# Kernel tuning notes

Hardware: AMD Instinct MI355X
Metric: run time of the kernel (lower is better)

Reference implementation:

```python
import jax, jax.numpy as jnp
import numpy as np

D = 512; H = 2048; NH = 8; NL = 6; VX = 32000; VY = 32000
B = 256; SX = 15; SY = 17; PAD = 0; DH = D // NH


def _pe_table(seq_len, d):
    pos = np.arange(seq_len, dtype=np.float32)[:, None]
    div = 1.0 / (10000.0 ** (np.arange(0, d, 2, dtype=np.float32) / d))
    pe = np.zeros((seq_len, d), dtype=np.float32)
    pe[:, 0::2] = np.sin(pos * div)
    pe[:, 1::2] = np.cos(pos * div)
    return jnp.asarray(pe)


def _ln(x, g, b, eps=1e-5):
    m = x.mean(-1, keepdims=True)
    v = ((x - m) ** 2).mean(-1, keepdims=True)
    return g * (x - m) / jnp.sqrt(v + eps) + b


def _attn(xq, xkv, mask, w, b):
    # w: [4, D, D] (q,k,v,o), b: [4, D]; mask broadcastable to [B,NH,Sq,Sk]
    bs, sq, _ = xq.shape
    sk = xkv.shape[1]
    q = (xq @ w[0] + b[0]).reshape(bs, sq, NH, DH).transpose(0, 2, 1, 3)
    k = (xkv @ w[1] + b[1]).reshape(bs, sk, NH, DH).transpose(0, 2, 1, 3)
    v = (xkv @ w[2] + b[2]).reshape(bs, sk, NH, DH).transpose(0, 2, 1, 3)
    s = jnp.einsum('bhqd,bhkd->bhqk', q, k) / np.sqrt(float(DH))
    s = jnp.where(mask == 0.0, -1e9, s)
    p = jax.nn.softmax(s, axis=-1)
    o = jnp.einsum('bhqk,bhkd->bhqd', p, v).transpose(0, 2, 1, 3).reshape(bs, sq, D)
    return o @ w[3] + b[3]


def setup_inputs():
    key = jax.random.key(0)
    ks = jax.random.split(key, 24)
    s = 0.02
    x = jax.random.randint(ks[0], (B, SX), 0, VX)
    y = jax.random.randint(ks[1], (B, SY), 0, VY)
    emb_x = (jax.random.normal(ks[2], (VX, D)) * s).at[PAD].set(0.0)
    emb_y = (jax.random.normal(ks[3], (VY, D)) * s).at[PAD].set(0.0)
    inp = dict(x=x, y=y, emb_x=emb_x, emb_y=emb_y)
    inp['enc_attn_w'] = jax.random.normal(ks[4], (NL, 4, D, D)) * s
    inp['enc_attn_b'] = jnp.zeros((NL, 4, D))
    inp['enc_ln'] = jnp.stack([jnp.ones((NL, 2, D)), jnp.zeros((NL, 2, D))], axis=2)  # [NL,2,2,D] (g,b)
    inp['enc_ffn_w0'] = jax.random.normal(ks[5], (NL, D, H)) * s
    inp['enc_ffn_b0'] = jnp.zeros((NL, H))
    inp['enc_ffn_w1'] = jax.random.normal(ks[6], (NL, H, D)) * s
    inp['enc_ffn_b1'] = jnp.zeros((NL, D))
    inp['dec_attn_w'] = jax.random.normal(ks[7], (NL, 8, D, D)) * s  # self q,k,v,o then cross q,k,v,o
    inp['dec_attn_b'] = jnp.zeros((NL, 8, D))
    inp['dec_ln'] = jnp.stack([jnp.ones((NL, 3, D)), jnp.zeros((NL, 3, D))], axis=2)  # [NL,3,2,D]
    inp['dec_ffn_w0'] = jax.random.normal(ks[8], (NL, D, H)) * s
    inp['dec_ffn_b0'] = jnp.zeros((NL, H))
    inp['dec_ffn_w1'] = jax.random.normal(ks[9], (NL, H, D)) * s
    inp['dec_ffn_b1'] = jnp.zeros((NL, D))
    inp['fc_w'] = jax.random.normal(ks[10], (D, VY)) * s
    inp['fc_b'] = jnp.zeros((VY,))
    return inp


def reference(x, y, emb_x, emb_y, enc_attn_w, enc_attn_b, enc_ln,
              enc_ffn_w0, enc_ffn_b0, enc_ffn_w1, enc_ffn_b1,
              dec_attn_w, dec_attn_b, dec_ln,
              dec_ffn_w0, dec_ffn_b0, dec_ffn_w1, dec_ffn_b1,
              fc_w, fc_b):
    pe = _pe_table(max(SX, SY + 1), D)
    mask_x = (x != PAD).astype(jnp.float32)[:, None, None, :]        # [B,1,1,SX]
    mask_pad = (y != PAD).astype(jnp.float32)[:, None, None, :]       # [B,1,1,SY]
    mask_y = mask_pad * jnp.tril(jnp.ones((SY, SY), jnp.float32))     # [B,1,SY,SY]

    hx = emb_x[x] + pe[:SX]
    for i in range(NL):
        a = _attn(hx, hx, mask_x, enc_attn_w[i], enc_attn_b[i])
        h0 = _ln(hx + a, enc_ln[i, 0, 0], enc_ln[i, 0, 1])
        f = jax.nn.relu(h0 @ enc_ffn_w0[i] + enc_ffn_b0[i]) @ enc_ffn_w1[i] + enc_ffn_b1[i]
        hx = _ln(h0 + f, enc_ln[i, 1, 0], enc_ln[i, 1, 1])

    hy = emb_y[y] + pe[:SY]
    for i in range(NL):
        a = _attn(hy, hy, mask_y, dec_attn_w[i, :4], dec_attn_b[i, :4])
        h0 = _ln(hy + a, dec_ln[i, 0, 0], dec_ln[i, 0, 1])
        c = _attn(h0, hx, mask_x, dec_attn_w[i, 4:], dec_attn_b[i, 4:])
        h1 = _ln(h0 + c, dec_ln[i, 1, 0], dec_ln[i, 1, 1])
        f = jax.nn.relu(h1 @ dec_ffn_w0[i] + dec_ffn_b0[i]) @ dec_ffn_w1[i] + dec_ffn_b1[i]
        hy = _ln(h1 + f, dec_ln[i, 2, 0], dec_ln[i, 2, 1])

    return hy @ fc_w + fc_b  # [B, SY, VY]
```

## Files before the change

### kernel.cpp

```cpp
#include <hip/hip_runtime.h>
#include <hip/hip_bf16.h>
#include <stdint.h>
#include <type_traits>

typedef __hip_bfloat16 bf16;
typedef __attribute__((ext_vector_type(8))) short bf16x8;
typedef __attribute__((ext_vector_type(4))) float f32x4;

#define DMODEL 512
#define HFF    2048
#define NHEADS 8
#define NLAYERS 6
#define DHEAD  64
#define BATCH  256
#define SXLEN  15
#define SYLEN  17

__device__ __forceinline__ float us2f(unsigned short u) {
  union { unsigned int i; float f; } c; c.i = ((unsigned int)u) << 16; return c.f;
}
__device__ __forceinline__ unsigned short f2us(float f) {
  bf16 h = __float2bfloat16(f);
  return *reinterpret_cast<unsigned short*>(&h);
}
__device__ __forceinline__ float b2f(bf16 v) { return __bfloat162float(v); }

__device__ __forceinline__ void gload_lds16(const void* g, void* l) {
  __builtin_amdgcn_global_load_lds(
      (const __attribute__((address_space(1))) unsigned int*)g,
      (__attribute__((address_space(3))) unsigned int*)l, 16, 0, 0);
}

template<int RELU, int MT, int NT, int WM, int WN, int ZMAP, int BIAS, typename OT>
__global__ __launch_bounds__(WM * WN * 64) void gemm_t(
    const bf16* __restrict__ A, const bf16* __restrict__ Wt,
    const float* __restrict__ bias, OT* __restrict__ C,
    int M, int N, int K, int ldk,
    long long wStride, long long bStride, long long cStride)
{
  constexpr int BK  = 64;
  constexpr int TH  = WM * WN * 64;
  constexpr int RB  = BK * 2;
  constexpr int MF  = MT / WM / 16;
  constexpr int NF  = NT / WN / 16;
  constexpr int WRS = MT / WM;
  constexpr int WCS = NT / WN;
  constexpr int ABY = MT * RB;
  constexpr int BBY = NT * RB;

  const int z = blockIdx.z;
  long long koff = 0;
  if (ZMAP == 1) {
    int idx = (z >> 1) * 8 + 5 + (z & 1);
    Wt   += (long long)idx * wStride;
    bias += (long long)idx * bStride;
  } else if (ZMAP == 2) {
    koff = (long long)z * K;
  } else {
    Wt   += (long long)z * wStride;
    bias += (long long)z * bStride;
  }
  C += (long long)z * cStride;

  __shared__ __align__(16) char lds[ABY + BBY];
  const int t    = threadIdx.x;
  const int m0   = blockIdx.y * MT, n0 = blockIdx.x * NT;
  const int wid  = t >> 6, lane = t & 63;
  const int wm   = wid / WN, wn = wid % WN;
  const int g    = lane >> 4, r = lane & 15;

  f32x4 acc[MF][NF];
  #pragma unroll
  for (int i = 0; i < MF; ++i)
    #pragma unroll
    for (int j = 0; j < NF; ++j) acc[i][j] = (f32x4)0.f;

  const char* Ab = (const char*)(A  + (long long)m0 * ldk + koff);
  const char* Bb = (const char*)(Wt + (long long)n0 * ldk + koff);
  const int rowBytes = ldk * 2;
  const int rdsw = (r & 7) << 4;

  for (int kt = 0; kt < K; kt += BK) {
    __syncthreads();
    #pragma unroll
    for (int off = 0; off < ABY; off += TH * 16) {
      int o = off + t * 16;
      int row = o >> 7, cb = (o & 127) ^ ((row & 7) << 4);
      gload_lds16(Ab + (long long)row * rowBytes + kt * 2 + cb, lds + o);
    }
    #pragma unroll
    for (int off = 0; off < BBY; off += TH * 16) {
      int o = off + t * 16;
      int row = o >> 7, cb = (o & 127) ^ ((row & 7) << 4);
      gload_lds16(Bb + (long long)row * rowBytes + kt * 2 + cb, lds + ABY + o);
    }
    __syncthreads();

    #pragma unroll
    for (int kh = 0; kh < BK / 32; ++kh) {
      bf16x8 af[MF], bfr[NF];
      #pragma unroll
      for (int ms = 0; ms < MF; ++ms)
        af[ms] = *(const bf16x8*)(lds + (wm * WRS + ms * 16 + r) * RB + ((kh * 64 + g * 16) ^ rdsw));
      #pragma unroll
      for (int ns = 0; ns < NF; ++ns)
        bfr[ns] = *(const bf16x8*)(lds + ABY + (wn * WCS + ns * 16 + r) * RB + ((kh * 64 + g * 16) ^ rdsw));
      #pragma unroll
      for (int ms = 0; ms < MF; ++ms)
        #pragma unroll
        for (int ns = 0; ns < NF; ++ns)
          acc[ms][ns] = __builtin_amdgcn_mfma_f32_16x16x32_bf16(af[ms], bfr[ns], acc[ms][ns], 0, 0, 0);
    }
  }

  #pragma unroll
  for (int ms = 0; ms < MF; ++ms) {
    int rowb = m0 + wm * WRS + ms * 16 + g * 4;
    #pragma unroll
    for (int ns = 0; ns < NF; ++ns) {
      int col = n0 + wn * WCS + ns * 16 + r;
      float bv = BIAS ? bias[col] : 0.f;
      f32x4 v = acc[ms][ns];
      #pragma unroll
      for (int j = 0; j < 4; ++j) {
        float o = v[j] + bv;
        if (RELU) o = fmaxf(o, 0.f);
        if constexpr (std::is_same<OT, float>::value)
          C[(long long)(rowb + j) * N + col] = o;
        else
          C[(long long)(rowb + j) * N + col] = __float2bfloat16(o);
      }
    }
  }
}

__global__ __launch_bounds__(256) void transpose_cast2(
    const float* __restrict__ inA, const float* __restrict__ inB, int zSplit,
    bf16* __restrict__ out, int K, int N)
{
  __shared__ unsigned short tile[32][33];
  int z = blockIdx.z;
  const float* ip = (z < zSplit) ? inA + (long long)z * K * N
                                 : inB + (long long)(z - zSplit) * K * N;
  unsigned short* op = (unsigned short*)out + (long long)z * K * N;
  int nx = blockIdx.x * 32, ky = blockIdx.y * 32;
  int tx = threadIdx.x, ty = threadIdx.y;
  #pragma unroll
  for (int j = 0; j < 4; ++j)
    tile[ty + j * 8][tx] = f2us(ip[(long long)(ky + ty + j * 8) * N + nx + tx]);
  __syncthreads();
  #pragma unroll
  for (int j = 0; j < 4; ++j)
    op[(long long)(nx + ty + j * 8) * K + ky + tx] = tile[tx][ty + j * 8];
}

__global__ __launch_bounds__(64) void embed2_k(
    const int* __restrict__ xids, const int* __restrict__ yids,
    const float* __restrict__ ex, const float* __restrict__ ey,
    bf16* __restrict__ ox, bf16* __restrict__ oy)
{
  int row = blockIdx.x;
  const int* ids; const float* emb; bf16* out; int S;
  if (row < BATCH * SXLEN) { ids = xids; emb = ex; out = ox; S = SXLEN; }
  else { row -= BATCH * SXLEN; ids = yids; emb = ey; out = oy; S = SYLEN; }
  int s = row % S;
  int lane = threadIdx.x;
  int id = ids[row];
  const float* e = emb + (long long)id * DMODEL;
  unsigned short* o = (unsigned short*)(out + (long long)row * DMODEL);
  #pragma unroll
  for (int j = 0; j < 8; ++j) {
    int d  = lane * 8 + j;
    int jj = d >> 1;
    float freq = __expf(-(float)(2 * jj) * (9.210340371976184f / 512.f));
    float ang  = (float)s * freq;
    float pe   = (d & 1) ? cosf(ang) : sinf(ang);
    o[d] = f2us(e[d] + pe);
  }
}

template<int CAUSAL>
__global__ __launch_bounds__(64) void attn_core(
    const bf16* __restrict__ Q, const bf16* __restrict__ Kk, const bf16* __restrict__ V,
    const int* __restrict__ tok, bf16* __restrict__ O, int Sq, int Sk)
{
  int bh = blockIdx.x; int b = bh >> 3; int h = bh & 7;
  __shared__ float Qs[SYLEN][DHEAD + 1], Ks[SYLEN][DHEAD + 1], Vs[SYLEN][DHEAD + 1];
  __shared__ float P[SYLEN][SYLEN + 1];
  __shared__ float msk[SYLEN];
  int t = threadIdx.x;

  for (int idx = t; idx < Sq * DHEAD; idx += 64) {
    int q = idx >> 6, d = idx & 63;
    Qs[q][d] = b2f(Q[((long long)(b * Sq + q)) * DMODEL + h * DHEAD + d]);
  }
  for (int idx = t; idx < Sk * DHEAD; idx += 64) {
    int k = idx >> 6, d = idx & 63;
    Ks[k][d] = b2f(Kk[((long long)(b * Sk + k)) * DMODEL + h * DHEAD + d]);
    Vs[k][d] = b2f(V [((long long)(b * Sk + k)) * DMODEL + h * DHEAD + d]);
  }
  if (t < Sk) msk[t] = (tok[b * Sk + t] != 0) ? 1.f : 0.f;
  __syncthreads();

  for (int idx = t; idx < Sq * Sk; idx += 64) {
    int q = idx / Sk, k = idx - q * Sk;
    float s = 0.f;
    #pragma unroll
    for (int i = 0; i < DHEAD; ++i) s += Qs[q][i] * Ks[k][i];
    s *= 0.125f;
    bool m = (msk[k] != 0.f) && (!CAUSAL || k <= q);
    P[q][k] = m ? s : -1e9f;
  }
  __syncthreads();

  if (t < Sq) {
    float mx = -1e30f;
    for (int k = 0; k < Sk; ++k) mx = fmaxf(mx, P[t][k]);
    float sum = 0.f;
    for (int k = 0; k < Sk; ++k) { float e = __expf(P[t][k] - mx); P[t][k] = e; sum += e; }
    float inv = 1.f / sum;
    for (int k = 0; k < Sk; ++k) P[t][k] *= inv;
  }
  __syncthreads();

  int d = t;
  for (int q = 0; q < Sq; ++q) {
    float o = 0.f;
    for (int k = 0; k < Sk; ++k) o += P[q][k] * Vs[k][d];
    O[((long long)(b * Sq + q)) * DMODEL + h * DHEAD + d] = __float2bfloat16(o);
  }
}

__global__ __launch_bounds__(64) void add_ln_k(
    const bf16* __restrict__ a, const bf16* __restrict__ b,
    const float* __restrict__ gam, const float* __restrict__ bet,
    bf16* __restrict__ out)
{
  long long row = blockIdx.x;
  int lane = threadIdx.x;
  union { uint4 u; unsigned short s[8]; } ua, ub, uo;
  ua.u = ((const uint4*)(a + row * DMODEL))[lane];
  ub.u = ((const uint4*)(b + row * DMODEL))[lane];
  float x[8]; float s = 0.f, sq = 0.f;
  #pragma unroll
  for (int j = 0; j < 8; ++j) {
    x[j] = us2f(ua.s[j]) + us2f(ub.s[j]);
    s += x[j]; sq += x[j] * x[j];
  }
  #pragma unroll
  for (int o = 32; o > 0; o >>= 1) { s += __shfl_xor(s, o); sq += __shfl_xor(sq, o); }
  float mean = s * (1.f / DMODEL);
  float var  = sq * (1.f / DMODEL) - mean * mean;
  float inv  = rsqrtf(var + 1e-5f);
  float4 g0 = ((const float4*)gam)[lane * 2], g1 = ((const float4*)gam)[lane * 2 + 1];
  float4 b0 = ((const float4*)bet)[lane * 2], b1 = ((const float4*)bet)[lane * 2 + 1];
  float gg[8] = {g0.x, g0.y, g0.z, g0.w, g1.x, g1.y, g1.z, g1.w};
  float bb[8] = {b0.x, b0.y, b0.z, b0.w, b1.x, b1.y, b1.z, b1.w};
  #pragma unroll
  for (int j = 0; j < 8; ++j)
    uo.s[j] = f2us(gg[j] * (x[j] - mean) * inv + bb[j]);
  ((uint4*)(out + row * DMODEL))[lane] = uo.u;
}

__global__ __launch_bounds__(64) void add_ln3_k(
    const bf16* __restrict__ R, const float* __restrict__ P, long long pStride,
    const float* __restrict__ bias,
    const float* __restrict__ gam, const float* __restrict__ bet,
    bf16* __restrict__ out)
{
  long long row = blockIdx.x;
  int lane = threadIdx.x;
  union { uint4 u; unsigned short s[8]; } ua, uo;
  ua.u = ((const uint4*)(R + row * DMODEL))[lane];
  const float4* p0 = (const float4*)(P + row * DMODEL);
  const float4* p1 = (const float4*)(P + pStride + row * DMODEL);
  float4 a0 = p0[lane * 2], a1 = p0[lane * 2 + 1];
  float4 c0 = p1[lane * 2], c1 = p1[lane * 2 + 1];
  float4 bi0 = ((const float4*)bias)[lane * 2], bi1 = ((const float4*)bias)[lane * 2 + 1];
  float pa[8] = {a0.x, a0.y, a0.z, a0.w, a1.x, a1.y, a1.z, a1.w};
  float pc[8] = {c0.x, c0.y, c0.z, c0.w, c1.x, c1.y, c1.z, c1.w};
  float pb[8] = {bi0.x, bi0.y, bi0.z, bi0.w, bi1.x, bi1.y, bi1.z, bi1.w};
  float x[8]; float s = 0.f, sq = 0.f;
  #pragma unroll
  for (int j = 0; j < 8; ++j) {
    x[j] = us2f(ua.s[j]) + pa[j] + pc[j] + pb[j];
    s += x[j]; sq += x[j] * x[j];
  }
  #pragma unroll
  for (int o = 32; o > 0; o >>= 1) { s += __shfl_xor(s, o); sq += __shfl_xor(sq, o); }
  float mean = s * (1.f / DMODEL);
  float var  = sq * (1.f / DMODEL) - mean * mean;
  float inv  = rsqrtf(var + 1e-5f);
  float4 g0 = ((const float4*)gam)[lane * 2], g1 = ((const float4*)gam)[lane * 2 + 1];
  float4 b0 = ((const float4*)bet)[lane * 2], b1 = ((const float4*)bet)[lane * 2 + 1];
  float gg[8] = {g0.x, g0.y, g0.z, g0.w, g1.x, g1.y, g1.z, g1.w};
  float bb[8] = {b0.x, b0.y, b0.z, b0.w, b1.x, b1.y, b1.z, b1.w};
  #pragma unroll
  for (int j = 0; j < 8; ++j)
    uo.s[j] = f2us(gg[j] * (x[j] - mean) * inv + bb[j]);
  ((uint4*)(out + row * DMODEL))[lane] = uo.u;
}

extern "C" void kernel_launch(void* const* d_in, const int* in_sizes, int n_in,
                              void* d_out, int out_size, void* d_ws, size_t ws_size,
                              hipStream_t stream)
{
  const int*   x        = (const int*)  d_in[0];
  const int*   y        = (const int*)  d_in[1];
  const float* emb_x    = (const float*)d_in[2];
  const float* emb_y    = (const float*)d_in[3];
  const float* enc_attn_w = (const float*)d_in[4];
  const float* enc_attn_b = (const float*)d_in[5];
  const float* enc_ln     = (const float*)d_in[6];
  const float* enc_f0w    = (const float*)d_in[7];
  const float* enc_f0b    = (const float*)d_in[8];
  const float* enc_f1w    = (const float*)d_in[9];
  const float* enc_f1b    = (const float*)d_in[10];
  const float* dec_attn_w = (const float*)d_in[11];
  const float* dec_attn_b = (const float*)d_in[12];
  const float* dec_ln     = (const float*)d_in[13];
  const float* dec_f0w    = (const float*)d_in[14];
  const float* dec_f0b    = (const float*)d_in[15];
  const float* dec_f1w    = (const float*)d_in[16];
  const float* dec_f1b    = (const float*)d_in[17];
  const float* fc_w       = (const float*)d_in[18];
  const float* fc_b       = (const float*)d_in[19];

  const int MX = BATCH * SXLEN;
  const int MY = BATCH * SYLEN;
  const long long DD = (long long)DMODEL * DMODEL;
  const long long SMEL = (long long)MY * DMODEL;
  const long long MXEL = (long long)MX * DMODEL;
  const long long FFEL = (long long)DMODEL * HFF;

  char* p = (char*)d_ws;
  auto alloc = [&](long long elems) -> bf16* {
    bf16* r = (bf16*)p; p += ((elems * 2 + 255) / 256) * 256; return r;
  };
  bf16* wt_attn = alloc(72 * DD);
  bf16* wt_f0   = alloc(12 * FFEL);
  bf16* wt_f1   = alloc(12 * FFEL);
  bf16* wt_fc   = alloc(32000LL * DMODEL);
  bf16* hx  = alloc(SMEL);
  bf16* hy  = alloc(SMEL);
  bf16* qb  = alloc(3 * SMEL);
  bf16* ao  = alloc(SMEL);
  bf16* h0  = alloc(SMEL);
  bf16* h1  = alloc(SMEL);
  bf16* mid = alloc((long long)MY * HFF);
  bf16* ckv = alloc(12 * MXEL);
  float* fp = (float*)alloc(2LL * MY * DMODEL * 2);
  if ((size_t)(p - (char*)d_ws) > ws_size) return;

  bf16* wt_enc_attn = wt_attn;
  bf16* wt_dec_attn = wt_attn + 24 * DD;
  bf16* wt_enc_f0   = wt_f0;
  bf16* wt_dec_f0   = wt_f0 + 6 * FFEL;
  bf16* wt_enc_f1   = wt_f1;
  bf16* wt_dec_f1   = wt_f1 + 6 * FFEL;

  dim3 tb(32, 8);
  transpose_cast2<<<dim3(16, 16, 72), tb, 0, stream>>>(enc_attn_w, dec_attn_w, 24, wt_attn, DMODEL, DMODEL);
  transpose_cast2<<<dim3(64, 16, 12), tb, 0, stream>>>(enc_f0w, dec_f0w, 6, wt_f0, DMODEL, HFF);
  transpose_cast2<<<dim3(16, 64, 12), tb, 0, stream>>>(enc_f1w, dec_f1w, 6, wt_f1, HFF, DMODEL);
  transpose_cast2<<<dim3(1000, 16, 1), tb, 0, stream>>>(fc_w, fc_w, 1, wt_fc, DMODEL, 32000);

  embed2_k<<<MX + MY, 64, 0, stream>>>(x, y, emb_x, emb_y, hx, hy);

  for (int i = 0; i < NLAYERS; ++i) {
    const bf16*  Wl = wt_enc_attn + (long long)i * 4 * DD;
    const float* Bl = enc_attn_b + (long long)i * 4 * DMODEL;
    const float* Lg = enc_ln + (size_t)i * 2048;
    gemm_t<0, 64, 64, 2, 1, 0, 1, bf16><<<dim3(8, 60, 3), 128, 0, stream>>>(hx, Wl, Bl, qb,
        MX, DMODEL, DMODEL, DMODEL, DD, DMODEL, SMEL);
    attn_core<0><<<BATCH * NHEADS, 64, 0, stream>>>(qb, qb + SMEL, qb + 2 * SMEL, x, ao, SXLEN, SXLEN);
    gemm_t<0, 64, 64, 2, 1, 0, 1, bf16><<<dim3(8, 60, 1), 128, 0, stream>>>(ao, Wl + 3 * DD, Bl + 3 * DMODEL, h1,
        MX, DMODEL, DMODEL, DMODEL, 0, 0, 0);
    add_ln_k<<<MX, 64, 0, stream>>>(hx, h1, Lg, Lg + 512, h0);
    gemm_t<1, 128, 128, 2, 2, 0, 1, bf16><<<dim3(16, 30, 1), 256, 0, stream>>>(h0,
        wt_enc_f0 + (long long)i * FFEL, enc_f0b + (long long)i * HFF, mid,
        MX, HFF, DMODEL, DMODEL, 0, 0, 0);
    gemm_t<0, 64, 64, 2, 1, 2, 0, float><<<dim3(8, 60, 2), 128, 0, stream>>>(mid,
        wt_enc_f1 + (long long)i * FFEL, enc_f1b, fp,
        MX, DMODEL, 1024, HFF, 0, 0, (long long)MY * DMODEL);
    add_ln3_k<<<MX, 64, 0, stream>>>(h0, fp, (long long)MY * DMODEL,
        enc_f1b + (long long)i * DMODEL, Lg + 1024, Lg + 1536, hx);
  }

  gemm_t<0, 64, 64, 2, 1, 1, 1, bf16><<<dim3(8, 60, 12), 128, 0, stream>>>(hx, wt_dec_attn,
      dec_attn_b, ckv, MX, DMODEL, DMODEL, DMODEL, DD, DMODEL, MXEL);

  for (int i = 0; i < NLAYERS; ++i) {
    const bf16*  Wl = wt_dec_attn + (long long)i * 8 * DD;
    const float* Bl = dec_attn_b + (long long)i * 8 * DMODEL;
    const float* Lg = dec_ln + (size_t)i * 3072;
    gemm_t<0, 64, 64, 2, 1, 0, 1, bf16><<<dim3(8, 68, 3), 128, 0, stream>>>(hy, Wl, Bl, qb,
        MY, DMODEL, DMODEL, DMODEL, DD, DMODEL, SMEL);
    attn_core<1><<<BATCH * NHEADS, 64, 0, stream>>>(qb, qb + SMEL, qb + 2 * SMEL, y, ao, SYLEN, SYLEN);
    gemm_t<0, 64, 64, 2, 1, 0, 1, bf16><<<dim3(8, 68, 1), 128, 0, stream>>>(ao, Wl + 3 * DD, Bl + 3 * DMODEL, h1,
        MY, DMODEL, DMODEL, DMODEL, 0, 0, 0);
    add_ln_k<<<MY, 64, 0, stream>>>(hy, h1, Lg, Lg + 512, h0);
    gemm_t<0, 64, 64, 2, 1, 0, 1, bf16><<<dim3(8, 68, 1), 128, 0, stream>>>(h0, Wl + 4 * DD, Bl + 4 * DMODEL, qb,
        MY, DMODEL, DMODEL, DMODEL, 0, 0, 0);
    attn_core<0><<<BATCH * NHEADS, 64, 0, stream>>>(qb, ckv + (long long)(2 * i) * MXEL,
        ckv + (long long)(2 * i + 1) * MXEL, x, ao, SYLEN, SXLEN);
    gemm_t<0, 64, 64, 2, 1, 0, 1, bf16><<<dim3(8, 68, 1), 128, 0, stream>>>(ao, Wl + 7 * DD, Bl + 7 * DMODEL, h1,
        MY, DMODEL, DMODEL, DMODEL, 0, 0, 0);
    add_ln_k<<<MY, 64, 0, stream>>>(h0, h1, Lg + 1024, Lg + 1536, h0);
    gemm_t<1, 128, 128, 2, 2, 0, 1, bf16><<<dim3(16, 34, 1), 256, 0, stream>>>(h0,
        wt_dec_f0 + (long long)i * FFEL, dec_f0b + (long long)i * HFF, mid,
        MY, HFF, DMODEL, DMODEL, 0, 0, 0);
    gemm_t<0, 64, 64, 2, 1, 2, 0, float><<<dim3(8, 68, 2), 128, 0, stream>>>(mid,
        wt_dec_f1 + (long long)i * FFEL, dec_f1b, fp,
        MY, DMODEL, 1024, HFF, 0, 0, (long long)MY * DMODEL);
    add_ln3_k<<<MY, 64, 0, stream>>>(h0, fp, (long long)MY * DMODEL,
        dec_f1b + (long long)i * DMODEL, Lg + 2048, Lg + 2560, hy);
  }

  gemm_t<0, 128, 256, 2, 4, 0, 1, float><<<dim3(125, 34, 1), 512, 0, stream>>>(hy, wt_fc, fc_b,
      (float*)d_out, MY, 32000, DMODEL, DMODEL, 0, 0, 0);
}
```

Measured before the change: 1.906 ms.

## Fuse LayerNorm into following GEMM prologue and residual add into GEMM epilogue

Residual adds move into the epilogue of the output-projection and FFN2 GEMMs. The LayerNorm moves into the prologue of the next GEMM: the full 512-wide A rows are loaded into LDS once, normalized there, and block (0,z=0) writes the normalized rows out for later residual use. This removes the separate add_ln kernels, the split-K FFN2 with its fp32 partial buffer, and several launches. In exchange the LNA GEMMs use much more LDS, every column block recomputes the row statistics, and the FFN1 and final FC tile shapes change (FFN1 now 64x64).

```diff
diff --git a/kernel.cpp b/kernel.cpp
--- a/kernel.cpp
+++ b/kernel.cpp
@@ -31,43 +31,45 @@
       (__attribute__((address_space(3))) unsigned int*)l, 16, 0, 0);
 }
 
-template<int RELU, int MT, int NT, int WM, int WN, int ZMAP, int BIAS, typename OT>
+template<int RELU, int MT, int NT, int WM, int WN, int ZMAP, int BIAS,
+         int LNA, int WRN, int RES, typename OT>
 __global__ __launch_bounds__(WM * WN * 64) void gemm_t(
     const bf16* __restrict__ A, const bf16* __restrict__ Wt,
     const float* __restrict__ bias, OT* __restrict__ C,
     int M, int N, int K, int ldk,
-    long long wStride, long long bStride, long long cStride)
+    long long wStride, long long bStride, long long cStride,
+    const float* __restrict__ lnG, const float* __restrict__ lnB,
+    bf16* __restrict__ normOut, const bf16* __restrict__ resid)
 {
   constexpr int BK  = 64;
   constexpr int TH  = WM * WN * 64;
   constexpr int RB  = BK * 2;
+  constexpr int ARB = LNA ? 1024 : RB;
   constexpr int MF  = MT / WM / 16;
   constexpr int NF  = NT / WN / 16;
   constexpr int WRS = MT / WM;
   constexpr int WCS = NT / WN;
-  constexpr int ABY = MT * RB;
+  constexpr int ABY = LNA ? MT * 1024 : MT * RB;
   constexpr int BBY = NT * RB;
 
   const int z = blockIdx.z;
-  long long koff = 0;
   if (ZMAP == 1) {
     int idx = (z >> 1) * 8 + 5 + (z & 1);
     Wt   += (long long)idx * wStride;
     bias += (long long)idx * bStride;
-  } else if (ZMAP == 2) {
-    koff = (long long)z * K;
   } else {
     Wt   += (long long)z * wStride;
     bias += (long long)z * bStride;
   }
   C += (long long)z * cStride;
 
-  __shared__ __align__(16) char lds[ABY + BBY];
+  __shared__ __align__(16) char lds[ABY + BBY + (LNA ? MT * 8 : 16)];
   const int t    = threadIdx.x;
   const int m0   = blockIdx.y * MT, n0 = blockIdx.x * NT;
   const int wid  = t >> 6, lane = t & 63;
   const int wm   = wid / WN, wn = wid % WN;
   const int g    = lane >> 4, r = lane & 15;
+  const int rdsw = (r & 7) << 4;
 
   f32x4 acc[MF][NF];
   #pragma unroll
@@ -75,18 +77,72 @@
     #pragma unroll
     for (int j = 0; j < NF; ++j) acc[i][j] = (f32x4)0.f;
 
-  const char* Ab = (const char*)(A  + (long long)m0 * ldk + koff);
-  const char* Bb = (const char*)(Wt + (long long)n0 * ldk + koff);
+  const char* Ab = (const char*)(A  + (long long)m0 * ldk);
+  const char* Bb = (const char*)(Wt + (long long)n0 * ldk);
   const int rowBytes = ldk * 2;
-  const int rdsw = (r & 7) << 4;
+
+  if constexpr (LNA) {
+    #pragma unroll
+    for (int off = 0; off < ABY; off += TH * 16) {
+      int o = off + t * 16;
+      int row = o >> 10, cb = o & 1023;
+      gload_lds16(Ab + (long long)row * rowBytes + (cb ^ ((row & 7) << 4)), lds + o);
+    }
+    __syncthreads();
+    constexpr int tpr = TH / MT;
+    constexpr int seg = 1024 / tpr;
+    const int rid = t / tpr, part = t % tpr;
+    const int base = rid * 1024 + part * seg;
+    float s = 0.f, sq = 0.f;
+    #pragma unroll 4
+    for (int i = 0; i < seg; i += 16) {
+      union { bf16x8 v; unsigned short u[8]; } c;
+      c.v = *(const bf16x8*)(lds + base + i);
+      #pragma unroll
+      for (int j = 0; j < 8; ++j) { float f = us2f(c.u[j]); s += f; sq += f * f; }
+    }
+    #pragma unroll
+    for (int m = 1; m < tpr; m <<= 1) { s += __shfl_xor(s, m); sq += __shfl_xor(sq, m); }
+    float* st = (float*)(lds + ABY + BBY);
+    if (part == 0) {
+      float mean = s * (1.f / 512.f);
+      float var  = sq * (1.f / 512.f) - mean * mean;
+      st[rid * 2] = mean; st[rid * 2 + 1] = rsqrtf(var + 1e-5f);
+    }
+    __syncthreads();
+    {
+      float mean = st[rid * 2], rstd = st[rid * 2 + 1];
+      const int wsw = (rid & 7) << 4;
+      #pragma unroll 4
+      for (int i = 0; i < seg; i += 16) {
+        int o  = base + i;
+        int cb = o & 1023;
+        int tc = (cb ^ wsw) >> 1;
+        float4 g0 = *(const float4*)(lnG + tc), g1 = *(const float4*)(lnG + tc + 4);
+        float4 b0 = *(const float4*)(lnB + tc), b1 = *(const float4*)(lnB + tc + 4);
+        float gg[8] = {g0.x, g0.y, g0.z, g0.w, g1.x, g1.y, g1.z, g1.w};
+        float bb[8] = {b0.x, b0.y, b0.z, b0.w, b1.x, b1.y, b1.z, b1.w};
+        union { bf16x8 v; unsigned short u[8]; } c, ov;
+        c.v = *(const bf16x8*)(lds + o);
+        #pragma unroll
+        for (int j = 0; j < 8; ++j)
+          ov.u[j] = f2us(gg[j] * (us2f(c.u[j]) - mean) * rstd + bb[j]);
+        *(bf16x8*)(lds + o) = ov.v;
+        if (WRN && blockIdx.x == 0 && z == 0)
+          *(bf16x8*)((char*)normOut + (long long)(m0 + rid) * 1024 + (cb ^ wsw)) = ov.v;
+      }
+    }
+  }
 
   for (int kt = 0; kt < K; kt += BK) {
     __syncthreads();
-    #pragma unroll
-    for (int off = 0; off < ABY; off += TH * 16) {
-      int o = off + t * 16;
-      int row = o >> 7, cb = (o & 127) ^ ((row & 7) << 4);
-      gload_lds16(Ab + (long long)row * rowBytes + kt * 2 + cb, lds + o);
+    if constexpr (!LNA) {
+      #pragma unroll
+      for (int off = 0; off < ABY; off += TH * 16) {
+        int o = off + t * 16;
+        int row = o >> 7, cb = (o & 127) ^ ((row & 7) << 4);
+        gload_lds16(Ab + (long long)row * rowBytes + kt * 2 + cb, lds + o);
+      }
     }
     #pragma unroll
     for (int off = 0; off < BBY; off += TH * 16) {
@@ -98,13 +154,16 @@
 
     #pragma unroll
     for (int kh = 0; kh < BK / 32; ++kh) {
+      const int akoff = LNA ? kt * 2 : 0;
       bf16x8 af[MF], bfr[NF];
       #pragma unroll
       for (int ms = 0; ms < MF; ++ms)
-        af[ms] = *(const bf16x8*)(lds + (wm * WRS + ms * 16 + r) * RB + ((kh * 64 + g * 16) ^ rdsw));
+        af[ms] = *(const bf16x8*)(lds + (wm * WRS + ms * 16 + r) * ARB
+                                      + ((akoff + kh * 64 + g * 16) ^ rdsw));
       #pragma unroll
       for (int ns = 0; ns < NF; ++ns)
-        bfr[ns] = *(const bf16x8*)(lds + ABY + (wn * WCS + ns * 16 + r) * RB + ((kh * 64 + g * 16) ^ rdsw));
+        bfr[ns] = *(const bf16x8*)(lds + ABY + (wn * WCS + ns * 16 + r) * RB
+                                       + ((kh * 64 + g * 16) ^ rdsw));
       #pragma unroll
       for (int ms = 0; ms < MF; ++ms)
         #pragma unroll
@@ -124,6 +183,8 @@
       #pragma unroll
       for (int j = 0; j < 4; ++j) {
         float o = v[j] + bv;
+        if (RES)
+          o += us2f(((const unsigned short*)resid)[(long long)(rowb + j) * 512 + col]);
         if (RELU) o = fmaxf(o, 0.f);
         if constexpr (std::is_same<OT, float>::value)
           C[(long long)(rowb + j) * N + col] = o;
@@ -231,59 +292,19 @@
   }
 }
 
-__global__ __launch_bounds__(64) void add_ln_k(
-    const bf16* __restrict__ a, const bf16* __restrict__ b,
-    const float* __restrict__ gam, const float* __restrict__ bet,
-    bf16* __restrict__ out)
-{
-  long long row = blockIdx.x;
-  int lane = threadIdx.x;
-  union { uint4 u; unsigned short s[8]; } ua, ub, uo;
-  ua.u = ((const uint4*)(a + row * DMODEL))[lane];
-  ub.u = ((const uint4*)(b + row * DMODEL))[lane];
-  float x[8]; float s = 0.f, sq = 0.f;
-  #pragma unroll
-  for (int j = 0; j < 8; ++j) {
-    x[j] = us2f(ua.s[j]) + us2f(ub.s[j]);
-    s += x[j]; sq += x[j] * x[j];
-  }
-  #pragma unroll
-  for (int o = 32; o > 0; o >>= 1) { s += __shfl_xor(s, o); sq += __shfl_xor(sq, o); }
-  float mean = s * (1.f / DMODEL);
-  float var  = sq * (1.f / DMODEL) - mean * mean;
-  float inv  = rsqrtf(var + 1e-5f);
-  float4 g0 = ((const float4*)gam)[lane * 2], g1 = ((const float4*)gam)[lane * 2 + 1];
-  float4 b0 = ((const float4*)bet)[lane * 2], b1 = ((const float4*)bet)[lane * 2 + 1];
-  float gg[8] = {g0.x, g0.y, g0.z, g0.w, g1.x, g1.y, g1.z, g1.w};
-  float bb[8] = {b0.x, b0.y, b0.z, b0.w, b1.x, b1.y, b1.z, b1.w};
-  #pragma unroll
-  for (int j = 0; j < 8; ++j)
-    uo.s[j] = f2us(gg[j] * (x[j] - mean) * inv + bb[j]);
-  ((uint4*)(out + row * DMODEL))[lane] = uo.u;
-}
-
-__global__ __launch_bounds__(64) void add_ln3_k(
-    const bf16* __restrict__ R, const float* __restrict__ P, long long pStride,
-    const float* __restrict__ bias,
+__global__ __launch_bounds__(64) void ln_k(
+    const bf16* __restrict__ xin,
     const float* __restrict__ gam, const float* __restrict__ bet,
     bf16* __restrict__ out)
 {
   long long row = blockIdx.x;
   int lane = threadIdx.x;
   union { uint4 u; unsigned short s[8]; } ua, uo;
-  ua.u = ((const uint4*)(R + row * DMODEL))[lane];
-  const float4* p0 = (const float4*)(P + row * DMODEL);
-  const float4* p1 = (const float4*)(P + pStride + row * DMODEL);
-  float4 a0 = p0[lane * 2], a1 = p0[lane * 2 + 1];
-  float4 c0 = p1[lane * 2], c1 = p1[lane * 2 + 1];
-  float4 bi0 = ((const float4*)bias)[lane * 2], bi1 = ((const float4*)bias)[lane * 2 + 1];
-  float pa[8] = {a0.x, a0.y, a0.z, a0.w, a1.x, a1.y, a1.z, a1.w};
-  float pc[8] = {c0.x, c0.y, c0.z, c0.w, c1.x, c1.y, c1.z, c1.w};
-  float pb[8] = {bi0.x, bi0.y, bi0.z, bi0.w, bi1.x, bi1.y, bi1.z, bi1.w};
+  ua.u = ((const uint4*)(xin + row * DMODEL))[lane];
   float x[8]; float s = 0.f, sq = 0.f;
   #pragma unroll
   for (int j = 0; j < 8; ++j) {
-    x[j] = us2f(ua.s[j]) + pa[j] + pc[j] + pb[j];
+    x[j] = us2f(ua.s[j]);
     s += x[j]; sq += x[j] * x[j];
   }
   #pragma unroll
@@ -345,11 +366,16 @@
   bf16* hy  = alloc(SMEL);
   bf16* qb  = alloc(3 * SMEL);
   bf16* ao  = alloc(SMEL);
-  bf16* h0  = alloc(SMEL);
-  bf16* h1  = alloc(SMEL);
   bf16* mid = alloc((long long)MY * HFF);
   bf16* ckv = alloc(12 * MXEL);
-  float* fp = (float*)alloc(2LL * MY * DMODEL * 2);
+  bf16* xh0 = alloc(SMEL);
+  bf16* h0n = alloc(SMEL);
+  bf16* xh1 = alloc(SMEL);
+  bf16* h1n = alloc(SMEL);
+  bf16* xhx = alloc(SMEL);
+  bf16* hxn = alloc(SMEL);
+  bf16* xhy = alloc(SMEL);
+  bf16* hyn = alloc(SMEL);
   if ((size_t)(p - (char*)d_ws) > ws_size) return;
 
   bf16* wt_enc_attn = wt_attn;
@@ -371,52 +397,69 @@
     const bf16*  Wl = wt_enc_attn + (long long)i * 4 * DD;
     const float* Bl = enc_attn_b + (long long)i * 4 * DMODEL;
     const float* Lg = enc_ln + (size_t)i * 2048;
-    gemm_t<0, 64, 64, 2, 1, 0, 1, bf16><<<dim3(8, 60, 3), 128, 0, stream>>>(hx, Wl, Bl, qb,
-        MX, DMODEL, DMODEL, DMODEL, DD, DMODEL, SMEL);
+    if (i == 0)
+      gemm_t<0, 64, 64, 2, 1, 0, 1, 0, 0, 0, bf16><<<dim3(8, 60, 3), 128, 0, stream>>>(
+          hx, Wl, Bl, qb, MX, DMODEL, DMODEL, DMODEL, DD, DMODEL, SMEL,
+          nullptr, nullptr, nullptr, nullptr);
+    else {
+      const float* Pg = enc_ln + (size_t)(i - 1) * 2048 + 1024;
+      gemm_t<0, 64, 64, 2, 1, 0, 1, 1, 1, 0, bf16><<<dim3(8, 60, 3), 128, 0, stream>>>(
+          xhx, Wl, Bl, qb, MX, DMODEL, DMODEL, DMODEL, DD, DMODEL, SMEL,
+          Pg, Pg + 512, hxn, nullptr);
+    }
     attn_core<0><<<BATCH * NHEADS, 64, 0, stream>>>(qb, qb + SMEL, qb + 2 * SMEL, x, ao, SXLEN, SXLEN);
-    gemm_t<0, 64, 64, 2, 1, 0, 1, bf16><<<dim3(8, 60, 1), 128, 0, stream>>>(ao, Wl + 3 * DD, Bl + 3 * DMODEL, h1,
-        MX, DMODEL, DMODEL, DMODEL, 0, 0, 0);
-    add_ln_k<<<MX, 64, 0, stream>>>(hx, h1, Lg, Lg + 512, h0);
-    gemm_t<1, 128, 128, 2, 2, 0, 1, bf16><<<dim3(16, 30, 1), 256, 0, stream>>>(h0,
-        wt_enc_f0 + (long long)i * FFEL, enc_f0b + (long long)i * HFF, mid,
-        MX, HFF, DMODEL, DMODEL, 0, 0, 0);
-    gemm_t<0, 64, 64, 2, 1, 2, 0, float><<<dim3(8, 60, 2), 128, 0, stream>>>(mid,
-        wt_enc_f1 + (long long)i * FFEL, enc_f1b, fp,
-        MX, DMODEL, 1024, HFF, 0, 0, (long long)MY * DMODEL);
-    add_ln3_k<<<MX, 64, 0, stream>>>(h0, fp, (long long)MY * DMODEL,
-        enc_f1b + (long long)i * DMODEL, Lg + 1024, Lg + 1536, hx);
-  }
-
-  gemm_t<0, 64, 64, 2, 1, 1, 1, bf16><<<dim3(8, 60, 12), 128, 0, stream>>>(hx, wt_dec_attn,
-      dec_attn_b, ckv, MX, DMODEL, DMODEL, DMODEL, DD, DMODEL, MXEL);
+    gemm_t<0, 64, 64, 2, 1, 0, 1, 0, 0, 1, bf16><<<dim3(8, 60, 1), 128, 0, stream>>>(
+        ao, Wl + 3 * DD, Bl + 3 * DMODEL, xh0, MX, DMODEL, DMODEL, DMODEL, 0, 0, 0,
+        nullptr, nullptr, nullptr, (i == 0 ? hx : hxn));
+    gemm_t<1, 64, 64, 2, 1, 0, 1, 1, 1, 0, bf16><<<dim3(32, 60, 1), 128, 0, stream>>>(
+        xh0, wt_enc_f0 + (long long)i * FFEL, enc_f0b + (long long)i * HFF, mid,
+        MX, HFF, DMODEL, DMODEL, 0, 0, 0, Lg, Lg + 512, h0n, nullptr);
+    gemm_t<0, 64, 64, 2, 1, 0, 1, 0, 0, 1, bf16><<<dim3(8, 60, 1), 128, 0, stream>>>(
+        mid, wt_enc_f1 + (long long)i * FFEL, enc_f1b + (long long)i * DMODEL, xhx,
+        MX, DMODEL, HFF, HFF, 0, 0, 0, nullptr, nullptr, nullptr, h0n);
+  }
+  ln_k<<<MX, 64, 0, stream>>>(xhx, enc_ln + 5 * 2048 + 1024, enc_ln + 5 * 2048 + 1536, hxn);
+
+  gemm_t<0, 64, 64, 2, 1, 1, 1, 0, 0, 0, bf16><<<dim3(8, 60, 12), 128, 0, stream>>>(
+      hxn, wt_dec_attn, dec_attn_b, ckv, MX, DMODEL, DMODEL, DMODEL, DD, DMODEL, MXEL,
+      nullptr, nullptr, nullptr, nullptr);
 
   for (int i = 0; i < NLAYERS; ++i) {
     const bf16*  Wl = wt_dec_attn + (long long)i * 8 * DD;
     const float* Bl = dec_attn_b + (long long)i * 8 * DMODEL;
     const float* Lg = dec_ln + (size_t)i * 3072;
-    gemm_t<0, 64, 64, 2, 1, 0, 1, bf16><<<dim3(8, 68, 3), 128, 0, stream>>>(hy, Wl, Bl, qb,
-        MY, DMODEL, DMODEL, DMODEL, DD, DMODEL, SMEL);
+    if (i == 0)
+      gemm_t<0, 64, 64, 2, 1, 0, 1, 0, 0, 0, bf16><<<dim3(8, 68, 3), 128, 0, stream>>>(
+          hy, Wl, Bl, qb, MY, DMODEL, DMODEL, DMODEL, DD, DMODEL, SMEL,
+          nullptr, nullptr, nullptr, nullptr);
+    else {
+      const float* Pg = dec_ln + (size_t)(i - 1) * 3072 + 2048;
+      gemm_t<0, 64, 64, 2, 1, 0, 1, 1, 1, 0, bf16><<<dim3(8, 68, 3), 128, 0, stream>>>(
+          xhy, Wl, Bl, qb, MY, DMODEL, DMODEL, DMODEL, DD, DMODEL, SMEL,
+          Pg, Pg + 512, hyn, nullptr);
+    }
     attn_core<1><<<BATCH * NHEADS, 64, 0, stream>>>(qb, qb + SMEL, qb + 2 * SMEL, y, ao, SYLEN, SYLEN);
-    gemm_t<0, 64, 64, 2, 1, 0, 1, bf16><<<dim3(8, 68, 1), 128, 0, stream>>>(ao, Wl + 3 * DD, Bl + 3 * DMODEL, h1,
-        MY, DMODEL, DMODEL, DMODEL, 0, 0, 0);
-    add_ln_k<<<MY, 64, 0, stream>>>(hy, h1, Lg, Lg + 512, h0);
-    gemm_t<0, 64, 64, 2, 1, 0, 1, bf16><<<dim3(8, 68, 1), 128, 0, stream>>>(h0, Wl + 4 * DD, Bl + 4 * DMODEL, qb,
-        MY, DMODEL, DMODEL, DMODEL, 0, 0, 0);
+    gemm_t<0, 64, 64, 2, 1, 0, 1, 0, 0, 1, bf16><<<dim3(8, 68, 1), 128, 0, stream>>>(
+        ao, Wl + 3 * DD, Bl + 3 * DMODEL, xh0, MY, DMODEL, DMODEL, DMODEL, 0, 0, 0,
+        nullptr, nullptr, nullptr, (i == 0 ? hy : hyn));
+    gemm_t<0, 64, 64, 2, 1, 0, 1, 1, 1, 0, bf16><<<dim3(8, 68, 1), 128, 0, stream>>>(
+        xh0, Wl + 4 * DD, Bl + 4 * DMODEL, qb, MY, DMODEL, DMODEL, DMODEL, 0, 0, 0,
+        Lg, Lg + 512, h0n, nullptr);
     attn_core<0><<<BATCH * NHEADS, 64, 0, stream>>>(qb, ckv + (long long)(2 * i) * MXEL,
         ckv + (long long)(2 * i + 1) * MXEL, x, ao, SYLEN, SXLEN);
-    gemm_t<0, 64, 64, 2, 1, 0, 1, bf16><<<dim3(8, 68, 1), 128, 0, stream>>>(ao, Wl + 7 * DD, Bl + 7 * DMODEL, h1,
-        MY, DMODEL, DMODEL, DMODEL, 0, 0, 0);
-    add_ln_k<<<MY, 64, 0, stream>>>(h0, h1, Lg + 1024, Lg + 1536, h0);
-    gemm_t<1, 128, 128, 2, 2, 0, 1, bf16><<<dim3(16, 34, 1), 256, 0, stream>>>(h0,
-        wt_dec_f0 + (long long)i * FFEL, dec_f0b + (long long)i * HFF, mid,
-        MY, HFF, DMODEL, DMODEL, 0, 0, 0);
-    gemm_t<0, 64, 64, 2, 1, 2, 0, float><<<dim3(8, 68, 2), 128, 0, stream>>>(mid,
-        wt_dec_f1 + (long long)i * FFEL, dec_f1b, fp,
-        MY, DMODEL, 1024, HFF, 0, 0, (long long)MY * DMODEL);
-    add_ln3_k<<<MY, 64, 0, stream>>>(h0, fp, (long long)MY * DMODEL,
-        dec_f1b + (long long)i * DMODEL, Lg + 2048, Lg + 2560, hy);
-  }
-
-  gemm_t<0, 128, 256, 2, 4, 0, 1, float><<<dim3(125, 34, 1), 512, 0, stream>>>(hy, wt_fc, fc_b,
-      (float*)d_out, MY, 32000, DMODEL, DMODEL, 0, 0, 0);
-}
+    gemm_t<0, 64, 64, 2, 1, 0, 1, 0, 0, 1, bf16><<<dim3(8, 68, 1), 128, 0, stream>>>(
+        ao, Wl + 7 * DD, Bl + 7 * DMODEL, xh1, MY, DMODEL, DMODEL, DMODEL, 0, 0, 0,
+        nullptr, nullptr, nullptr, h0n);
+    gemm_t<1, 64, 64, 2, 1, 0, 1, 1, 1, 0, bf16><<<dim3(32, 68, 1), 128, 0, stream>>>(
+        xh1, wt_dec_f0 + (long long)i * FFEL, dec_f0b + (long long)i * HFF, mid,
+        MY, HFF, DMODEL, DMODEL, 0, 0, 0, Lg + 1024, Lg + 1536, h1n, nullptr);
+    gemm_t<0, 64, 64, 2, 1, 0, 1, 0, 0, 1, bf16><<<dim3(8, 68, 1), 128, 0, stream>>>(
+        mid, wt_dec_f1 + (long long)i * FFEL, dec_f1b + (long long)i * DMODEL, xhy,
+        MY, DMODEL, HFF, HFF, 0, 0, 0, nullptr, nullptr, nullptr, h1n);
+  }
+  ln_k<<<MY, 64, 0, stream>>>(xhy, dec_ln + 5 * 3072 + 2048, dec_ln + 5 * 3072 + 2560, hyn);
+
+  gemm_t<0, 256, 128, 4, 2, 0, 1, 0, 0, 0, float><<<dim3(250, 17, 1), 512, 0, stream>>>(
+      hyn, wt_fc, fc_b, (float*)d_out, MY, 32000, DMODEL, DMODEL, 0, 0, 0,
+      nullptr, nullptr, nullptr, nullptr);
+}
```

Measured after the change: 3.644 ms. 1.91x slower.
